# Kernel optimization log

Measured on AMD Instinct MI355X. Metric: run time of the kernel, lower is better.

The kernel has to match this reference:

```python
import jax, jax.numpy as jnp
import numpy as np

KEY_DIM = 64
DENSE_DIM = 128
B, N, M = 8, 2048, 256


def setup_inputs() -> dict:
    key = jax.random.key(0)
    ks = jax.random.split(key, 10)
    s_in = 1.0 / np.sqrt(M)
    s_k = 1.0 / np.sqrt(KEY_DIM)
    s_d = 1.0 / np.sqrt(DENSE_DIM)
    return {
        "x": jax.random.normal(ks[0], (B, N, M), dtype=jnp.float32),
        "Wq": jax.random.normal(ks[1], (M, KEY_DIM), dtype=jnp.float32) * s_in,
        "Wk": jax.random.normal(ks[2], (M, KEY_DIM), dtype=jnp.float32) * s_in,
        "Wv": jax.random.normal(ks[3], (M, KEY_DIM), dtype=jnp.float32) * s_in,
        "W1": jax.random.normal(ks[4], (KEY_DIM, DENSE_DIM), dtype=jnp.float32) * s_k,
        "b1": jnp.zeros((DENSE_DIM,), dtype=jnp.float32),
        "W2": jax.random.normal(ks[5], (DENSE_DIM, DENSE_DIM), dtype=jnp.float32) * s_d,
        "b2": jnp.zeros((DENSE_DIM,), dtype=jnp.float32),
        "W3": jax.random.normal(ks[6], (DENSE_DIM, DENSE_DIM), dtype=jnp.float32) * s_d,
        "b3": jnp.zeros((DENSE_DIM,), dtype=jnp.float32),
    }


def reference(x, Wq, Wk, Wv, W1, b1, W2, b2, W3, b3):
    scale = np.sqrt(KEY_DIM).astype(np.float32)
    q = jnp.einsum('bnm,mk->bnk', x, Wq)
    k = jnp.einsum('bnm,mk->bnk', x, Wk)
    v = jnp.einsum('bnm,mk->bnk', x, Wv)
    scores = jnp.einsum('bik,bjk->bij', q, k) / scale  # [B, N, N]
    weights = jax.nn.softmax(scores, axis=-1)
    z = jnp.einsum('bij,bjk->bik', weights, v)  # [B, N, key_dim]
    h = jax.nn.elu(z @ W1 + b1)
    h = jax.nn.elu(h @ W2 + b2)
    out = jax.nn.elu(h @ W3 + b3)
    return out
```

## Files before the change

### kernel.cpp

```cpp
#include <hip/hip_runtime.h>
#include <cstdint>
#include <cstddef>

#define B_ 8
#define N_ 2048
#define M_ 256
#define KD 64
#define DD 128
#define BN (B_ * N_)
#define KSPLIT 4
#define KT_PER (N_ / 64 / KSPLIT)

typedef __attribute__((ext_vector_type(8))) short s16x8;
typedef __attribute__((ext_vector_type(4))) float f32x4;
typedef __attribute__((ext_vector_type(4))) unsigned int u32x4;

__device__ __forceinline__ float elu_f(float x) {
    return x > 0.f ? x : (__expf(x) - 1.f);
}

__device__ __forceinline__ unsigned short f2bf(float f) {
    unsigned int u = __float_as_uint(f);
    u = (u + 0x7FFFu + ((u >> 16) & 1u)) >> 16;
    return (unsigned short)u;
}
__device__ __forceinline__ float bf2f(unsigned short h) {
    return __uint_as_float((unsigned int)h << 16);
}
__device__ __forceinline__ unsigned short bflo(float f, unsigned short h) {
    return f2bf(f - bf2f(h));
}
__device__ __forceinline__ unsigned int packw(float f) {
    unsigned short h = f2bf(f);
    unsigned short lo = bflo(f, h);
    return (unsigned int)h | ((unsigned int)lo << 16);
}
__device__ __forceinline__ unsigned int bfpack2(float a, float b) {
    return (unsigned int)f2bf(a) | ((unsigned int)f2bf(b) << 16);
}
__device__ __forceinline__ float bflo32(unsigned int u) { return __uint_as_float(u << 16); }
__device__ __forceinline__ float bfhi32(unsigned int u) { return __uint_as_float(u & 0xffff0000u); }

__device__ __forceinline__ void unpack8(const unsigned int* ip, s16x8& ahi, s16x8& alo) {
    const uint4 u0 = *reinterpret_cast<const uint4*>(ip);
    const uint4 u1 = *reinterpret_cast<const uint4*>(ip + 4);
    u32x4 hv, lv;
    hv.x = __byte_perm(u0.x, u0.y, 0x5410);
    hv.y = __byte_perm(u0.z, u0.w, 0x5410);
    hv.z = __byte_perm(u1.x, u1.y, 0x5410);
    hv.w = __byte_perm(u1.z, u1.w, 0x5410);
    lv.x = __byte_perm(u0.x, u0.y, 0x7632);
    lv.y = __byte_perm(u0.z, u0.w, 0x7632);
    lv.z = __byte_perm(u1.x, u1.y, 0x7632);
    lv.w = __byte_perm(u1.z, u1.w, 0x7632);
    ahi = __builtin_bit_cast(s16x8, hv);
    alo = __builtin_bit_cast(s16x8, lv);
}

__global__ __launch_bounds__(256)
void pack_kernel(const float* __restrict__ Wq, const float* __restrict__ Wk,
                 const float* __restrict__ Wv, const float* __restrict__ W1,
                 const float* __restrict__ W2, const float* __restrict__ W3,
                 unsigned short* __restrict__ pQh, unsigned short* __restrict__ pQl,
                 unsigned short* __restrict__ pW1h, unsigned short* __restrict__ pW1l,
                 unsigned short* __restrict__ pW2h, unsigned short* __restrict__ pW2l,
                 unsigned short* __restrict__ pW3h, unsigned short* __restrict__ pW3l) {
    const int id = blockIdx.x * 256 + threadIdx.x;
    const float* W;
    unsigned short *ph, *pl;
    int ncol, ct, c, lane, base;
    if (id < 6144) {
        int mat = id >> 11, rem = id & 2047;
        ct = rem >> 9; c = (rem >> 6) & 7; lane = rem & 63;
        W = (mat == 0) ? Wq : (mat == 1) ? Wk : Wv;
        ncol = KD; ph = pQh; pl = pQl;
        base = (((mat * 4 + ct) * 8 + c) * 64 + lane) * 8;
    } else {
        int id2 = id - 6144;
        if (id2 < 1024) {
            ct = id2 >> 7; c = (id2 >> 6) & 1; lane = id2 & 63;
            W = W1; ncol = DD; ph = pW1h; pl = pW1l;
            base = ((ct * 2 + c) * 64 + lane) * 8;
        } else if (id2 < 3072) {
            int id3 = id2 - 1024;
            ct = id3 >> 8; c = (id3 >> 6) & 3; lane = id3 & 63;
            W = W2; ncol = DD; ph = pW2h; pl = pW2l;
            base = ((ct * 4 + c) * 64 + lane) * 8;
        } else {
            int id3 = id2 - 3072;
            ct = id3 >> 8; c = (id3 >> 6) & 3; lane = id3 & 63;
            W = W3; ncol = DD; ph = pW3h; pl = pW3l;
            base = ((ct * 4 + c) * 64 + lane) * 8;
        }
    }
    const int col = ct * 16 + (lane & 15);
    const int kb = c * 32 + (lane >> 4) * 8;
    #pragma unroll
    for (int j = 0; j < 8; ++j) {
        float v = W[(size_t)(kb + j) * ncol + col];
        unsigned short h = f2bf(v);
        ph[base + j] = h;
        pl[base + j] = bflo(v, h);
    }
}

__global__ __launch_bounds__(256)
void qkv_kernel(const float* __restrict__ x,
                const unsigned short* __restrict__ pQh,
                unsigned short* __restrict__ qb, unsigned short* __restrict__ kb,
                unsigned short* __restrict__ vtb) {
    __shared__ unsigned short xh[32 * 264];
    __shared__ float dbuf[32 * 204];
    const int t = threadIdx.x;
    const int row0 = blockIdx.x * 32;

    for (int i = t; i < 2048; i += 256) {
        int rr = i >> 6, c4 = i & 63;
        float4 v = reinterpret_cast<const float4*>(x + (size_t)(row0 + rr) * M_)[c4];
        ushort4 o;
        o.x = f2bf(v.x); o.y = f2bf(v.y); o.z = f2bf(v.z); o.w = f2bf(v.w);
        *reinterpret_cast<ushort4*>(&xh[rr * 264 + c4 * 4]) = o;
    }
    __syncthreads();

    const int w = t >> 6, l = t & 63, g = l >> 4, r = l & 15;
    const int t0 = 3 * w, t1 = 3 * w + 1, t2 = 3 * w + 2;

    f32x4 acc[3][2];
    #pragma unroll
    for (int m = 0; m < 3; ++m)
        #pragma unroll
        for (int s = 0; s < 2; ++s)
            acc[m][s] = (f32x4){0.f, 0.f, 0.f, 0.f};

    #pragma unroll
    for (int c = 0; c < 8; ++c) {
        const s16x8 a0 = *reinterpret_cast<const s16x8*>(&xh[r * 264 + c * 32 + g * 8]);
        const s16x8 a1 = *reinterpret_cast<const s16x8*>(&xh[(16 + r) * 264 + c * 32 + g * 8]);
        const s16x8 b0 = *reinterpret_cast<const s16x8*>(pQh + ((t0 * 8 + c) * 64 + l) * 8);
        const s16x8 b1 = *reinterpret_cast<const s16x8*>(pQh + ((t1 * 8 + c) * 64 + l) * 8);
        const s16x8 b2 = *reinterpret_cast<const s16x8*>(pQh + ((t2 * 8 + c) * 64 + l) * 8);
        acc[0][0] = __builtin_amdgcn_mfma_f32_16x16x32_bf16(a0, b0, acc[0][0], 0, 0, 0);
        acc[0][1] = __builtin_amdgcn_mfma_f32_16x16x32_bf16(a1, b0, acc[0][1], 0, 0, 0);
        acc[1][0] = __builtin_amdgcn_mfma_f32_16x16x32_bf16(a0, b1, acc[1][0], 0, 0, 0);
        acc[1][1] = __builtin_amdgcn_mfma_f32_16x16x32_bf16(a1, b1, acc[1][1], 0, 0, 0);
        acc[2][0] = __builtin_amdgcn_mfma_f32_16x16x32_bf16(a0, b2, acc[2][0], 0, 0, 0);
        acc[2][1] = __builtin_amdgcn_mfma_f32_16x16x32_bf16(a1, b2, acc[2][1], 0, 0, 0);
    }

    {
        const int c0 = (t0 >> 2) * 68 + (t0 & 3) * 16 + r;
        const int c1 = (t1 >> 2) * 68 + (t1 & 3) * 16 + r;
        const int c2 = (t2 >> 2) * 68 + (t2 & 3) * 16 + r;
        #pragma unroll
        for (int s = 0; s < 2; ++s)
            #pragma unroll
            for (int reg = 0; reg < 4; ++reg) {
                const int rw = (s * 16 + 4 * g + reg) * 204;
                dbuf[rw + c0] = acc[0][s][reg];
                dbuf[rw + c1] = acc[1][s][reg];
                dbuf[rw + c2] = acc[2][s][reg];
            }
    }
    __syncthreads();

    const int b = row0 >> 11, n0 = row0 & 2047;
    {
        const int mat = t >> 7, rem = t & 127, rr = rem >> 2, cq = rem & 3;
        const float* src = &dbuf[rr * 204 + mat * 68 + cq * 16];
        float4 v0 = *reinterpret_cast<const float4*>(src);
        float4 v1 = *reinterpret_cast<const float4*>(src + 4);
        float4 v2 = *reinterpret_cast<const float4*>(src + 8);
        float4 v3 = *reinterpret_cast<const float4*>(src + 12);
        const float sc = (mat == 0) ? 0.125f : 1.0f;
        uint4 o0, o1;
        o0.x = bfpack2(v0.x * sc, v0.y * sc);
        o0.y = bfpack2(v0.z * sc, v0.w * sc);
        o0.z = bfpack2(v1.x * sc, v1.y * sc);
        o0.w = bfpack2(v1.z * sc, v1.w * sc);
        o1.x = bfpack2(v2.x * sc, v2.y * sc);
        o1.y = bfpack2(v2.z * sc, v2.w * sc);
        o1.z = bfpack2(v3.x * sc, v3.y * sc);
        o1.w = bfpack2(v3.z * sc, v3.w * sc);
        unsigned short* dst = (mat == 0 ? qb : kb) + (size_t)(row0 + rr) * KD + cq * 16;
        *reinterpret_cast<uint4*>(dst)     = o0;
        *reinterpret_cast<uint4*>(dst + 8) = o1;
    }
    {
        const int d = t >> 2, ng = (t & 3) * 8;
        unsigned short tmp[8];
        #pragma unroll
        for (int i = 0; i < 8; ++i)
            tmp[i] = f2bf(dbuf[(ng + i) * 204 + 136 + d]);
        uint4 o0;
        o0.x = (unsigned)tmp[0] | ((unsigned)tmp[1] << 16);
        o0.y = (unsigned)tmp[2] | ((unsigned)tmp[3] << 16);
        o0.z = (unsigned)tmp[4] | ((unsigned)tmp[5] << 16);
        o0.w = (unsigned)tmp[6] | ((unsigned)tmp[7] << 16);
        *reinterpret_cast<uint4*>(vtb + ((size_t)b * KD + d) * N_ + n0 + ng) = o0;
    }
}

__global__ __launch_bounds__(128)
void attn_kernel(const unsigned short* __restrict__ qb,
                 const unsigned short* __restrict__ kb,
                 const unsigned short* __restrict__ vtb,
                 unsigned short* __restrict__ Zp, float* __restrict__ lsum) {
    __shared__ __align__(16) unsigned short ks[64 * 72];
    __shared__ __align__(16) unsigned short vt[64 * 72];

    const int t = threadIdx.x;
    const int w = t >> 6;
    const int l = t & 63;
    const int g = l >> 4;
    const int r = l & 15;
    const int bid = blockIdx.x;
    const int split = bid & 3;
    const int qt = (bid >> 2) & 31;
    const int bb = bid >> 7;
    const int qrow0 = qt * 64 + w * 32;
    const int k0 = split * (N_ / KSPLIT);

    const unsigned short* qrowA = qb + ((size_t)bb * N_ + qrow0 + r) * KD + g * 8;
    const unsigned short* qrowB = qrowA + (size_t)16 * KD;
    const s16x8 qfA0 = *reinterpret_cast<const s16x8*>(qrowA);
    const s16x8 qfA1 = *reinterpret_cast<const s16x8*>(qrowA + 32);
    const s16x8 qfB0 = *reinterpret_cast<const s16x8*>(qrowB);
    const s16x8 qfB1 = *reinterpret_cast<const s16x8*>(qrowB + 32);

    const unsigned short* kbase = kb + ((size_t)bb * N_ + k0) * KD;
    const unsigned short* vbase = vtb + (size_t)bb * KD * N_ + k0;

    for (int c = t; c < 512; c += 128) {
        const int row = c >> 3, sub = c & 7;
        *reinterpret_cast<s16x8*>(&ks[row * 72 + sub * 8]) =
            *reinterpret_cast<const s16x8*>(kbase + (size_t)row * KD + sub * 8);
        const s16x8 vv = *reinterpret_cast<const s16x8*>(vbase + (size_t)row * N_ + sub * 8);
        const u32x4 vw = __builtin_bit_cast(u32x4, vv);
        const int slot = 32 * (sub >> 2) + 16 * (sub & 1) + 4 * ((sub >> 1) & 1);
        *reinterpret_cast<uint2*>(&vt[row * 72 + slot])     = make_uint2(vw.x, vw.y);
        *reinterpret_cast<uint2*>(&vt[row * 72 + slot + 8]) = make_uint2(vw.z, vw.w);
    }
    __syncthreads();

    f32x4 zacA0 = {0.f,0.f,0.f,0.f}, zacA1 = {0.f,0.f,0.f,0.f};
    f32x4 zacA2 = {0.f,0.f,0.f,0.f}, zacA3 = {0.f,0.f,0.f,0.f};
    f32x4 zacB0 = {0.f,0.f,0.f,0.f}, zacB1 = {0.f,0.f,0.f,0.f};
    f32x4 zacB2 = {0.f,0.f,0.f,0.f}, zacB3 = {0.f,0.f,0.f,0.f};
    float laccA = 0.f, laccB = 0.f;

    for (int kt = 0; kt < KT_PER; ++kt) {
        s16x8 kr[4], vr[4];
        const bool pf = (kt + 1 < KT_PER);
        if (pf) {
            const unsigned short* kg = kbase + (size_t)(kt + 1) * 64 * KD;
            const unsigned short* vg = vbase + (size_t)(kt + 1) * 64;
            #pragma unroll
            for (int i = 0; i < 4; ++i) {
                const int c = t + 128 * i, row = c >> 3, sub = c & 7;
                kr[i] = *reinterpret_cast<const s16x8*>(kg + (size_t)row * KD + sub * 8);
                vr[i] = *reinterpret_cast<const s16x8*>(vg + (size_t)row * N_ + sub * 8);
            }
        }

        f32x4 sA[4], sB[4];
        #pragma unroll
        for (int i = 0; i < 4; ++i) { sA[i] = (f32x4){0,0,0,0}; sB[i] = (f32x4){0,0,0,0}; }
        {
            const s16x8 kf00 = *reinterpret_cast<const s16x8*>(&ks[(r +  0) * 72 + g * 8]);
            const s16x8 kf01 = *reinterpret_cast<const s16x8*>(&ks[(r +  0) * 72 + g * 8 + 32]);
            const s16x8 kf10 = *reinterpret_cast<const s16x8*>(&ks[(r + 16) * 72 + g * 8]);
            const s16x8 kf11 = *reinterpret_cast<const s16x8*>(&ks[(r + 16) * 72 + g * 8 + 32]);
            const s16x8 kf20 = *reinterpret_cast<const s16x8*>(&ks[(r + 32) * 72 + g * 8]);
            const s16x8 kf21 = *reinterpret_cast<const s16x8*>(&ks[(r + 32) * 72 + g * 8 + 32]);
            const s16x8 kf30 = *reinterpret_cast<const s16x8*>(&ks[(r + 48) * 72 + g * 8]);
            const s16x8 kf31 = *reinterpret_cast<const s16x8*>(&ks[(r + 48) * 72 + g * 8 + 32]);
            sA[0] = __builtin_amdgcn_mfma_f32_16x16x32_bf16(kf00, qfA0, sA[0], 0, 0, 0);
            sA[0] = __builtin_amdgcn_mfma_f32_16x16x32_bf16(kf01, qfA1, sA[0], 0, 0, 0);
            sA[1] = __builtin_amdgcn_mfma_f32_16x16x32_bf16(kf10, qfA0, sA[1], 0, 0, 0);
            sA[1] = __builtin_amdgcn_mfma_f32_16x16x32_bf16(kf11, qfA1, sA[1], 0, 0, 0);
            sA[2] = __builtin_amdgcn_mfma_f32_16x16x32_bf16(kf20, qfA0, sA[2], 0, 0, 0);
            sA[2] = __builtin_amdgcn_mfma_f32_16x16x32_bf16(kf21, qfA1, sA[2], 0, 0, 0);
            sA[3] = __builtin_amdgcn_mfma_f32_16x16x32_bf16(kf30, qfA0, sA[3], 0, 0, 0);
            sA[3] = __builtin_amdgcn_mfma_f32_16x16x32_bf16(kf31, qfA1, sA[3], 0, 0, 0);
            sB[0] = __builtin_amdgcn_mfma_f32_16x16x32_bf16(kf00, qfB0, sB[0], 0, 0, 0);
            sB[0] = __builtin_amdgcn_mfma_f32_16x16x32_bf16(kf01, qfB1, sB[0], 0, 0, 0);
            sB[1] = __builtin_amdgcn_mfma_f32_16x16x32_bf16(kf10, qfB0, sB[1], 0, 0, 0);
            sB[1] = __builtin_amdgcn_mfma_f32_16x16x32_bf16(kf11, qfB1, sB[1], 0, 0, 0);
            sB[2] = __builtin_amdgcn_mfma_f32_16x16x32_bf16(kf20, qfB0, sB[2], 0, 0, 0);
            sB[2] = __builtin_amdgcn_mfma_f32_16x16x32_bf16(kf21, qfB1, sB[2], 0, 0, 0);
            sB[3] = __builtin_amdgcn_mfma_f32_16x16x32_bf16(kf30, qfB0, sB[3], 0, 0, 0);
            sB[3] = __builtin_amdgcn_mfma_f32_16x16x32_bf16(kf31, qfB1, sB[3], 0, 0, 0);
        }

        unsigned int wA[8], wB[8];
        #pragma unroll
        for (int tt = 0; tt < 4; ++tt) {
            float p0 = __expf(sA[tt][0]);
            float p1 = __expf(sA[tt][1]);
            float p2 = __expf(sA[tt][2]);
            float p3 = __expf(sA[tt][3]);
            laccA += (p0 + p1) + (p2 + p3);
            wA[2 * tt]     = bfpack2(p0, p1);
            wA[2 * tt + 1] = bfpack2(p2, p3);
        }
        #pragma unroll
        for (int tt = 0; tt < 4; ++tt) {
            float p0 = __expf(sB[tt][0]);
            float p1 = __expf(sB[tt][1]);
            float p2 = __expf(sB[tt][2]);
            float p3 = __expf(sB[tt][3]);
            laccB += (p0 + p1) + (p2 + p3);
            wB[2 * tt]     = bfpack2(p0, p1);
            wB[2 * tt + 1] = bfpack2(p2, p3);
        }
        u32x4 pwA0 = {wA[0], wA[1], wA[2], wA[3]};
        u32x4 pwA1 = {wA[4], wA[5], wA[6], wA[7]};
        u32x4 pwB0 = {wB[0], wB[1], wB[2], wB[3]};
        u32x4 pwB1 = {wB[4], wB[5], wB[6], wB[7]};
        const s16x8 paA0 = __builtin_bit_cast(s16x8, pwA0);
        const s16x8 paA1 = __builtin_bit_cast(s16x8, pwA1);
        const s16x8 paB0 = __builtin_bit_cast(s16x8, pwB0);
        const s16x8 paB1 = __builtin_bit_cast(s16x8, pwB1);

        const s16x8 vf00 = *reinterpret_cast<const s16x8*>(&vt[(r +  0) * 72 + g * 8]);
        const s16x8 vf01 = *reinterpret_cast<const s16x8*>(&vt[(r +  0) * 72 + g * 8 + 32]);
        const s16x8 vf10 = *reinterpret_cast<const s16x8*>(&vt[(r + 16) * 72 + g * 8]);
        const s16x8 vf11 = *reinterpret_cast<const s16x8*>(&vt[(r + 16) * 72 + g * 8 + 32]);
        const s16x8 vf20 = *reinterpret_cast<const s16x8*>(&vt[(r + 32) * 72 + g * 8]);
        const s16x8 vf21 = *reinterpret_cast<const s16x8*>(&vt[(r + 32) * 72 + g * 8 + 32]);
        const s16x8 vf30 = *reinterpret_cast<const s16x8*>(&vt[(r + 48) * 72 + g * 8]);
        const s16x8 vf31 = *reinterpret_cast<const s16x8*>(&vt[(r + 48) * 72 + g * 8 + 32]);

        zacA0 = __builtin_amdgcn_mfma_f32_16x16x32_bf16(paA0, vf00, zacA0, 0, 0, 0);
        zacA0 = __builtin_amdgcn_mfma_f32_16x16x32_bf16(paA1, vf01, zacA0, 0, 0, 0);
        zacA1 = __builtin_amdgcn_mfma_f32_16x16x32_bf16(paA0, vf10, zacA1, 0, 0, 0);
        zacA1 = __builtin_amdgcn_mfma_f32_16x16x32_bf16(paA1, vf11, zacA1, 0, 0, 0);
        zacA2 = __builtin_amdgcn_mfma_f32_16x16x32_bf16(paA0, vf20, zacA2, 0, 0, 0);
        zacA2 = __builtin_amdgcn_mfma_f32_16x16x32_bf16(paA1, vf21, zacA2, 0, 0, 0);
        zacA3 = __builtin_amdgcn_mfma_f32_16x16x32_bf16(paA0, vf30, zacA3, 0, 0, 0);
        zacA3 = __builtin_amdgcn_mfma_f32_16x16x32_bf16(paA1, vf31, zacA3, 0, 0, 0);
        zacB0 = __builtin_amdgcn_mfma_f32_16x16x32_bf16(paB0, vf00, zacB0, 0, 0, 0);
        zacB0 = __builtin_amdgcn_mfma_f32_16x16x32_bf16(paB1, vf01, zacB0, 0, 0, 0);
        zacB1 = __builtin_amdgcn_mfma_f32_16x16x32_bf16(paB0, vf10, zacB1, 0, 0, 0);
        zacB1 = __builtin_amdgcn_mfma_f32_16x16x32_bf16(paB1, vf11, zacB1, 0, 0, 0);
        zacB2 = __builtin_amdgcn_mfma_f32_16x16x32_bf16(paB0, vf20, zacB2, 0, 0, 0);
        zacB2 = __builtin_amdgcn_mfma_f32_16x16x32_bf16(paB1, vf21, zacB2, 0, 0, 0);
        zacB3 = __builtin_amdgcn_mfma_f32_16x16x32_bf16(paB0, vf30, zacB3, 0, 0, 0);
        zacB3 = __builtin_amdgcn_mfma_f32_16x16x32_bf16(paB1, vf31, zacB3, 0, 0, 0);

        __syncthreads();
        if (pf) {
            #pragma unroll
            for (int i = 0; i < 4; ++i) {
                const int c = t + 128 * i, row = c >> 3, sub = c & 7;
                *reinterpret_cast<s16x8*>(&ks[row * 72 + sub * 8]) = kr[i];
                const u32x4 vw = __builtin_bit_cast(u32x4, vr[i]);
                const int slot = 32 * (sub >> 2) + 16 * (sub & 1) + 4 * ((sub >> 1) & 1);
                *reinterpret_cast<uint2*>(&vt[row * 72 + slot])     = make_uint2(vw.x, vw.y);
                *reinterpret_cast<uint2*>(&vt[row * 72 + slot + 8]) = make_uint2(vw.z, vw.w);
            }
        }
        __syncthreads();
    }

    const size_t rowbase = (size_t)split * BN + (size_t)bb * N_ + qrow0;
    {
        float ltA = laccA;
        ltA += __shfl_xor(ltA, 16);
        ltA += __shfl_xor(ltA, 32);
        float ltB = laccB;
        ltB += __shfl_xor(ltB, 16);
        ltB += __shfl_xor(ltB, 32);
        if (l < 16) {
            lsum[rowbase + r]      = ltA;
            lsum[rowbase + 16 + r] = ltB;
        }
    }
    #pragma unroll
    for (int reg = 0; reg < 4; ++reg) {
        unsigned short* zrA = Zp + (rowbase + 4 * g + reg) * KD + r;
        zrA[ 0] = f2bf(zacA0[reg]);
        zrA[16] = f2bf(zacA1[reg]);
        zrA[32] = f2bf(zacA2[reg]);
        zrA[48] = f2bf(zacA3[reg]);
        unsigned short* zrB = Zp + (rowbase + 16 + 4 * g + reg) * KD + r;
        zrB[ 0] = f2bf(zacB0[reg]);
        zrB[16] = f2bf(zacB1[reg]);
        zrB[32] = f2bf(zacB2[reg]);
        zrB[48] = f2bf(zacB3[reg]);
    }
}

__global__ __launch_bounds__(256)
void mlp_kernel(const unsigned short* __restrict__ Zp, const float* __restrict__ lsum,
                const unsigned short* __restrict__ pW1h, const unsigned short* __restrict__ pW1l,
                const unsigned short* __restrict__ pW2h, const unsigned short* __restrict__ pW2l,
                const unsigned short* __restrict__ pW3h, const unsigned short* __restrict__ pW3l,
                const float* __restrict__ b1, const float* __restrict__ b2,
                const float* __restrict__ b3, float* __restrict__ out) {
    __shared__ unsigned int zW[32 * 68];
    __shared__ unsigned int hW[32 * 140];
    const int t = threadIdx.x;
    const int row0 = blockIdx.x * 32;

    {
        const int rr = t >> 3, c8 = (t & 7) * 8;
        const size_t grow = (size_t)row0 + rr;
        const float inv = 1.0f / (lsum[grow] + lsum[BN + grow] +
                                  lsum[2 * (size_t)BN + grow] + lsum[3 * (size_t)BN + grow]);
        const size_t off = grow * KD + c8;
        const uint4 z0 = *reinterpret_cast<const uint4*>(Zp + off);
        const uint4 z1 = *reinterpret_cast<const uint4*>(Zp + (size_t)BN * KD + off);
        const uint4 z2 = *reinterpret_cast<const uint4*>(Zp + 2 * (size_t)BN * KD + off);
        const uint4 z3 = *reinterpret_cast<const uint4*>(Zp + 3 * (size_t)BN * KD + off);
        const unsigned int a0[4] = {z0.x, z0.y, z0.z, z0.w};
        const unsigned int a1[4] = {z1.x, z1.y, z1.z, z1.w};
        const unsigned int a2[4] = {z2.x, z2.y, z2.z, z2.w};
        const unsigned int a3[4] = {z3.x, z3.y, z3.z, z3.w};
        unsigned int ww[8];
        #pragma unroll
        for (int i = 0; i < 4; ++i) {
            float lo = bflo32(a0[i]) + bflo32(a1[i]) + bflo32(a2[i]) + bflo32(a3[i]);
            float hi = bfhi32(a0[i]) + bfhi32(a1[i]) + bfhi32(a2[i]) + bfhi32(a3[i]);
            ww[2 * i]     = packw(lo * inv);
            ww[2 * i + 1] = packw(hi * inv);
        }
        uint4 o0, o1;
        o0.x = ww[0]; o0.y = ww[1]; o0.z = ww[2]; o0.w = ww[3];
        o1.x = ww[4]; o1.y = ww[5]; o1.z = ww[6]; o1.w = ww[7];
        *reinterpret_cast<uint4*>(&zW[rr * 68 + c8])     = o0;
        *reinterpret_cast<uint4*>(&zW[rr * 68 + c8 + 4]) = o1;
    }
    __syncthreads();

    const int w = t >> 6, l = t & 63, g = l >> 4, r = l & 15;
    const int ctA = 2 * w, ctB = 2 * w + 1;

    f32x4 aA[2], aB[2];
    #pragma unroll
    for (int s = 0; s < 2; ++s) { aA[s] = (f32x4){0,0,0,0}; aB[s] = (f32x4){0,0,0,0}; }
    #pragma unroll
    for (int c = 0; c < 2; ++c) {
        s16x8 h0, l0, h1, l1;
        unpack8(&zW[r * 68 + c * 32 + g * 8], h0, l0);
        unpack8(&zW[(16 + r) * 68 + c * 32 + g * 8], h1, l1);
        const int baseA = ((ctA * 2 + c) * 64 + l) * 8;
        const int baseB = ((ctB * 2 + c) * 64 + l) * 8;
        const s16x8 bhA = *reinterpret_cast<const s16x8*>(pW1h + baseA);
        const s16x8 blA = *reinterpret_cast<const s16x8*>(pW1l + baseA);
        const s16x8 bhB = *reinterpret_cast<const s16x8*>(pW1h + baseB);
        const s16x8 blB = *reinterpret_cast<const s16x8*>(pW1l + baseB);
        aA[0] = __builtin_amdgcn_mfma_f32_16x16x32_bf16(h0, bhA, aA[0], 0, 0, 0);
        aA[0] = __builtin_amdgcn_mfma_f32_16x16x32_bf16(h0, blA, aA[0], 0, 0, 0);
        aA[0] = __builtin_amdgcn_mfma_f32_16x16x32_bf16(l0, bhA, aA[0], 0, 0, 0);
        aA[1] = __builtin_amdgcn_mfma_f32_16x16x32_bf16(h1, bhA, aA[1], 0, 0, 0);
        aA[1] = __builtin_amdgcn_mfma_f32_16x16x32_bf16(h1, blA, aA[1], 0, 0, 0);
        aA[1] = __builtin_amdgcn_mfma_f32_16x16x32_bf16(l1, bhA, aA[1], 0, 0, 0);
        aB[0] = __builtin_amdgcn_mfma_f32_16x16x32_bf16(h0, bhB, aB[0], 0, 0, 0);
        aB[0] = __builtin_amdgcn_mfma_f32_16x16x32_bf16(h0, blB, aB[0], 0, 0, 0);
        aB[0] = __builtin_amdgcn_mfma_f32_16x16x32_bf16(l0, bhB, aB[0], 0, 0, 0);
        aB[1] = __builtin_amdgcn_mfma_f32_16x16x32_bf16(h1, bhB, aB[1], 0, 0, 0);
        aB[1] = __builtin_amdgcn_mfma_f32_16x16x32_bf16(h1, blB, aB[1], 0, 0, 0);
        aB[1] = __builtin_amdgcn_mfma_f32_16x16x32_bf16(l1, bhB, aB[1], 0, 0, 0);
    }
    {
        const float bvA = b1[ctA * 16 + r], bvB = b1[ctB * 16 + r];
        #pragma unroll
        for (int s = 0; s < 2; ++s)
            #pragma unroll
            for (int reg = 0; reg < 4; ++reg) {
                const int rw = (s * 16 + 4 * g + reg) * 140;
                hW[rw + ctA * 16 + r] = packw(elu_f(aA[s][reg] + bvA));
                hW[rw + ctB * 16 + r] = packw(elu_f(aB[s][reg] + bvB));
            }
    }
    __syncthreads();

    #pragma unroll
    for (int s = 0; s < 2; ++s) { aA[s] = (f32x4){0,0,0,0}; aB[s] = (f32x4){0,0,0,0}; }
    #pragma unroll
    for (int c = 0; c < 4; ++c) {
        s16x8 h0, l0, h1, l1;
        unpack8(&hW[r * 140 + c * 32 + g * 8], h0, l0);
        unpack8(&hW[(16 + r) * 140 + c * 32 + g * 8], h1, l1);
        const int baseA = ((ctA * 4 + c) * 64 + l) * 8;
        const int baseB = ((ctB * 4 + c) * 64 + l) * 8;
        const s16x8 bhA = *reinterpret_cast<const s16x8*>(pW2h + baseA);
        const s16x8 blA = *reinterpret_cast<const s16x8*>(pW2l + baseA);
        const s16x8 bhB = *reinterpret_cast<const s16x8*>(pW2h + baseB);
        const s16x8 blB = *reinterpret_cast<const s16x8*>(pW2l + baseB);
        aA[0] = __builtin_amdgcn_mfma_f32_16x16x32_bf16(h0, bhA, aA[0], 0, 0, 0);
        aA[0] = __builtin_amdgcn_mfma_f32_16x16x32_bf16(h0, blA, aA[0], 0, 0, 0);
        aA[0] = __builtin_amdgcn_mfma_f32_16x16x32_bf16(l0, bhA, aA[0], 0, 0, 0);
        aA[1] = __builtin_amdgcn_mfma_f32_16x16x32_bf16(h1, bhA, aA[1], 0, 0, 0);
        aA[1] = __builtin_amdgcn_mfma_f32_16x16x32_bf16(h1, blA, aA[1], 0, 0, 0);
        aA[1] = __builtin_amdgcn_mfma_f32_16x16x32_bf16(l1, bhA, aA[1], 0, 0, 0);
        aB[0] = __builtin_amdgcn_mfma_f32_16x16x32_bf16(h0, bhB, aB[0], 0, 0, 0);
        aB[0] = __builtin_amdgcn_mfma_f32_16x16x32_bf16(h0, blB, aB[0], 0, 0, 0);
        aB[0] = __builtin_amdgcn_mfma_f32_16x16x32_bf16(l0, bhB, aB[0], 0, 0, 0);
        aB[1] = __builtin_amdgcn_mfma_f32_16x16x32_bf16(h1, bhB, aB[1], 0, 0, 0);
        aB[1] = __builtin_amdgcn_mfma_f32_16x16x32_bf16(h1, blB, aB[1], 0, 0, 0);
        aB[1] = __builtin_amdgcn_mfma_f32_16x16x32_bf16(l1, bhB, aB[1], 0, 0, 0);
    }
    __syncthreads();
    {
        const float bvA = b2[ctA * 16 + r], bvB = b2[ctB * 16 + r];
        #pragma unroll
        for (int s = 0; s < 2; ++s)
            #pragma unroll
            for (int reg = 0; reg < 4; ++reg) {
                const int rw = (s * 16 + 4 * g + reg) * 140;
                hW[rw + ctA * 16 + r] = packw(elu_f(aA[s][reg] + bvA));
                hW[rw + ctB * 16 + r] = packw(elu_f(aB[s][reg] + bvB));
            }
    }
    __syncthreads();

    #pragma unroll
    for (int s = 0; s < 2; ++s) { aA[s] = (f32x4){0,0,0,0}; aB[s] = (f32x4){0,0,0,0}; }
    #pragma unroll
    for (int c = 0; c < 4; ++c) {
        s16x8 h0, l0, h1, l1;
        unpack8(&hW[r * 140 + c * 32 + g * 8], h0, l0);
        unpack8(&hW[(16 + r) * 140 + c * 32 + g * 8], h1, l1);
        const int baseA = ((ctA * 4 + c) * 64 + l) * 8;
        const int baseB = ((ctB * 4 + c) * 64 + l) * 8;
        const s16x8 bhA = *reinterpret_cast<const s16x8*>(pW3h + baseA);
        const s16x8 blA = *reinterpret_cast<const s16x8*>(pW3l + baseA);
        const s16x8 bhB = *reinterpret_cast<const s16x8*>(pW3h + baseB);
        const s16x8 blB = *reinterpret_cast<const s16x8*>(pW3l + baseB);
        aA[0] = __builtin_amdgcn_mfma_f32_16x16x32_bf16(h0, bhA, aA[0], 0, 0, 0);
        aA[0] = __builtin_amdgcn_mfma_f32_16x16x32_bf16(h0, blA, aA[0], 0, 0, 0);
        aA[0] = __builtin_amdgcn_mfma_f32_16x16x32_bf16(l0, bhA, aA[0], 0, 0, 0);
        aA[1] = __builtin_amdgcn_mfma_f32_16x16x32_bf16(h1, bhA, aA[1], 0, 0, 0);
        aA[1] = __builtin_amdgcn_mfma_f32_16x16x32_bf16(h1, blA, aA[1], 0, 0, 0);
        aA[1] = __builtin_amdgcn_mfma_f32_16x16x32_bf16(l1, bhA, aA[1], 0, 0, 0);
        aB[0] = __builtin_amdgcn_mfma_f32_16x16x32_bf16(h0, bhB, aB[0], 0, 0, 0);
        aB[0] = __builtin_amdgcn_mfma_f32_16x16x32_bf16(h0, blB, aB[0], 0, 0, 0);
        aB[0] = __builtin_amdgcn_mfma_f32_16x16x32_bf16(l0, bhB, aB[0], 0, 0, 0);
        aB[1] = __builtin_amdgcn_mfma_f32_16x16x32_bf16(h1, bhB, aB[1], 0, 0, 0);
        aB[1] = __builtin_amdgcn_mfma_f32_16x16x32_bf16(h1, blB, aB[1], 0, 0, 0);
        aB[1] = __builtin_amdgcn_mfma_f32_16x16x32_bf16(l1, bhB, aB[1], 0, 0, 0);
    }
    {
        const float bvA = b3[ctA * 16 + r], bvB = b3[ctB * 16 + r];
        #pragma unroll
        for (int s = 0; s < 2; ++s)
            #pragma unroll
            for (int reg = 0; reg < 4; ++reg) {
                float* orow = out + (size_t)(row0 + s * 16 + 4 * g + reg) * DD;
                orow[ctA * 16 + r] = elu_f(aA[s][reg] + bvA);
                orow[ctB * 16 + r] = elu_f(aB[s][reg] + bvB);
            }
    }
}

extern "C" void kernel_launch(void* const* d_in, const int* in_sizes, int n_in,
                              void* d_out, int out_size, void* d_ws, size_t ws_size,
                              hipStream_t stream) {
    (void)in_sizes; (void)n_in; (void)out_size; (void)ws_size;
    const float* x  = (const float*)d_in[0];
    const float* Wq = (const float*)d_in[1];
    const float* Wk = (const float*)d_in[2];
    const float* Wv = (const float*)d_in[3];
    const float* W1 = (const float*)d_in[4];
    const float* b1 = (const float*)d_in[5];
    const float* W2 = (const float*)d_in[6];
    const float* b2 = (const float*)d_in[7];
    const float* W3 = (const float*)d_in[8];
    const float* b3 = (const float*)d_in[9];
    float* out = (float*)d_out;

    const size_t nt = (size_t)BN * KD;
    unsigned short* qbf = (unsigned short*)d_ws;
    unsigned short* kbf = qbf + nt;
    unsigned short* vtb = kbf + nt;
    unsigned short* Zp  = vtb + nt;
    float* lsum = (float*)(Zp + (size_t)KSPLIT * nt);
    unsigned short* pQh  = (unsigned short*)(lsum + (size_t)KSPLIT * BN);
    unsigned short* pQl  = pQh + 49152;
    unsigned short* pW1h = pQl + 49152;
    unsigned short* pW1l = pW1h + 8192;
    unsigned short* pW2h = pW1l + 8192;
    unsigned short* pW2l = pW2h + 16384;
    unsigned short* pW3h = pW2l + 16384;
    unsigned short* pW3l = pW3h + 16384;

    pack_kernel<<<dim3(44), 256, 0, stream>>>(Wq, Wk, Wv, W1, W2, W3,
                                              pQh, pQl, pW1h, pW1l, pW2h, pW2l, pW3h, pW3l);
    qkv_kernel<<<dim3(BN / 32), 256, 0, stream>>>(x, pQh, qbf, kbf, vtb);
    attn_kernel<<<dim3(BN / 64 * KSPLIT), 128, 0, stream>>>(qbf, kbf, vtb, Zp, lsum);
    mlp_kernel<<<dim3(BN / 32), 256, 0, stream>>>(Zp, lsum, pW1h, pW1l, pW2h, pW2l,
                                                  pW3h, pW3l, b1, b2, b3, out);
}
```

Baseline: 52.16 us.

## Split attention keys eight ways and use exp2 with log2e-prescaled queries

Doubles the key-dimension split of the attention kernel from 4 to 8, giving twice as many blocks with half the keys each, and generalizes the MLP-side merge of partial Z and row sums to loop over KSPLIT. Queries are prescaled by log2(e)/sqrt(d) so the softmax uses exp2f directly, saving a multiply per score. This aims for better occupancy and latency hiding, at the cost of twice the partial-result writes and reads in the merge step.

```diff
diff --git a/kernel.cpp b/kernel.cpp
--- a/kernel.cpp
+++ b/kernel.cpp
@@ -8,7 +8,7 @@
 #define KD 64
 #define DD 128
 #define BN (B_ * N_)
-#define KSPLIT 4
+#define KSPLIT 8
 #define KT_PER (N_ / 64 / KSPLIT)
 
 typedef __attribute__((ext_vector_type(8))) short s16x8;
@@ -172,7 +172,7 @@
         float4 v1 = *reinterpret_cast<const float4*>(src + 4);
         float4 v2 = *reinterpret_cast<const float4*>(src + 8);
         float4 v3 = *reinterpret_cast<const float4*>(src + 12);
-        const float sc = (mat == 0) ? 0.125f : 1.0f;
+        const float sc = (mat == 0) ? 0.18033688011112042f : 1.0f;
         uint4 o0, o1;
         o0.x = bfpack2(v0.x * sc, v0.y * sc);
         o0.y = bfpack2(v0.z * sc, v0.w * sc);
@@ -215,9 +215,9 @@
     const int g = l >> 4;
     const int r = l & 15;
     const int bid = blockIdx.x;
-    const int split = bid & 3;
-    const int qt = (bid >> 2) & 31;
-    const int bb = bid >> 7;
+    const int split = bid & 7;
+    const int qt = (bid >> 3) & 31;
+    const int bb = bid >> 8;
     const int qrow0 = qt * 64 + w * 32;
     const int k0 = split * (N_ / KSPLIT);
 
@@ -296,20 +296,20 @@
         unsigned int wA[8], wB[8];
         #pragma unroll
         for (int tt = 0; tt < 4; ++tt) {
-            float p0 = __expf(sA[tt][0]);
-            float p1 = __expf(sA[tt][1]);
-            float p2 = __expf(sA[tt][2]);
-            float p3 = __expf(sA[tt][3]);
+            float p0 = exp2f(sA[tt][0]);
+            float p1 = exp2f(sA[tt][1]);
+            float p2 = exp2f(sA[tt][2]);
+            float p3 = exp2f(sA[tt][3]);
             laccA += (p0 + p1) + (p2 + p3);
             wA[2 * tt]     = bfpack2(p0, p1);
             wA[2 * tt + 1] = bfpack2(p2, p3);
         }
         #pragma unroll
         for (int tt = 0; tt < 4; ++tt) {
-            float p0 = __expf(sB[tt][0]);
-            float p1 = __expf(sB[tt][1]);
-            float p2 = __expf(sB[tt][2]);
-            float p3 = __expf(sB[tt][3]);
+            float p0 = exp2f(sB[tt][0]);
+            float p1 = exp2f(sB[tt][1]);
+            float p2 = exp2f(sB[tt][2]);
+            float p3 = exp2f(sB[tt][3]);
             laccB += (p0 + p1) + (p2 + p3);
             wB[2 * tt]     = bfpack2(p0, p1);
             wB[2 * tt + 1] = bfpack2(p2, p3);
@@ -407,28 +407,27 @@
     {
         const int rr = t >> 3, c8 = (t & 7) * 8;
         const size_t grow = (size_t)row0 + rr;
-        const float inv = 1.0f / (lsum[grow] + lsum[BN + grow] +
-                                  lsum[2 * (size_t)BN + grow] + lsum[3 * (size_t)BN + grow]);
+        float lt = 0.f;
+        #pragma unroll
+        for (int s2 = 0; s2 < KSPLIT; ++s2)
+            lt += lsum[(size_t)s2 * BN + grow];
+        const float inv = 1.0f / lt;
         const size_t off = grow * KD + c8;
-        const uint4 z0 = *reinterpret_cast<const uint4*>(Zp + off);
-        const uint4 z1 = *reinterpret_cast<const uint4*>(Zp + (size_t)BN * KD + off);
-        const uint4 z2 = *reinterpret_cast<const uint4*>(Zp + 2 * (size_t)BN * KD + off);
-        const uint4 z3 = *reinterpret_cast<const uint4*>(Zp + 3 * (size_t)BN * KD + off);
-        const unsigned int a0[4] = {z0.x, z0.y, z0.z, z0.w};
-        const unsigned int a1[4] = {z1.x, z1.y, z1.z, z1.w};
-        const unsigned int a2[4] = {z2.x, z2.y, z2.z, z2.w};
-        const unsigned int a3[4] = {z3.x, z3.y, z3.z, z3.w};
-        unsigned int ww[8];
-        #pragma unroll
-        for (int i = 0; i < 4; ++i) {
-            float lo = bflo32(a0[i]) + bflo32(a1[i]) + bflo32(a2[i]) + bflo32(a3[i]);
-            float hi = bfhi32(a0[i]) + bfhi32(a1[i]) + bfhi32(a2[i]) + bfhi32(a3[i]);
-            ww[2 * i]     = packw(lo * inv);
-            ww[2 * i + 1] = packw(hi * inv);
+        float lo[4] = {0.f, 0.f, 0.f, 0.f};
+        float hi[4] = {0.f, 0.f, 0.f, 0.f};
+        #pragma unroll
+        for (int s2 = 0; s2 < KSPLIT; ++s2) {
+            const uint4 zv = *reinterpret_cast<const uint4*>(Zp + (size_t)s2 * BN * KD + off);
+            lo[0] += bflo32(zv.x); hi[0] += bfhi32(zv.x);
+            lo[1] += bflo32(zv.y); hi[1] += bfhi32(zv.y);
+            lo[2] += bflo32(zv.z); hi[2] += bfhi32(zv.z);
+            lo[3] += bflo32(zv.w); hi[3] += bfhi32(zv.w);
         }
         uint4 o0, o1;
-        o0.x = ww[0]; o0.y = ww[1]; o0.z = ww[2]; o0.w = ww[3];
-        o1.x = ww[4]; o1.y = ww[5]; o1.z = ww[6]; o1.w = ww[7];
+        o0.x = packw(lo[0] * inv); o0.y = packw(hi[0] * inv);
+        o0.z = packw(lo[1] * inv); o0.w = packw(hi[1] * inv);
+        o1.x = packw(lo[2] * inv); o1.y = packw(hi[2] * inv);
+        o1.z = packw(lo[3] * inv); o1.w = packw(hi[3] * inv);
         *reinterpret_cast<uint4*>(&zW[rr * 68 + c8])     = o0;
         *reinterpret_cast<uint4*>(&zW[rr * 68 + c8 + 4]) = o1;
     }
```

Result: slower. 60.27 us (+15.6%).
